# Performance work log

Hardware: AMD Instinct MI355X
Metric: run time of the kernel (lower is better)

## Reference

```python
import jax, jax.numpy as jnp
import numpy as np

B, S, DM, H = 2, 2048, 1024, 16
D = DM // H  # head dim = 64


def setup_inputs() -> dict:
    key = jax.random.key(0)
    k1, k2, k3, k4, k5 = jax.random.split(key, 5)
    hidden_states = jax.random.normal(k1, (B, S, DM), dtype=jnp.float32)
    attention_mask = jnp.zeros((B, 1, S, S), dtype=jnp.float32)
    position_ids = jnp.broadcast_to(jnp.arange(S, dtype=jnp.int32), (B, S))
    # nn.Linear weights stored as (out, in); x @ W.T
    Wq = jax.random.normal(k2, (DM, DM), dtype=jnp.float32) * 0.02
    Wk = jax.random.normal(k3, (DM, DM), dtype=jnp.float32) * 0.02
    Wv = jax.random.normal(k4, (DM, DM), dtype=jnp.float32) * 0.02
    return {"hidden_states": hidden_states, "attention_mask": attention_mask,
            "position_ids": position_ids, "Wq": Wq, "Wk": Wk, "Wv": Wv}


def _rotate_half(x):
    h = x.shape[-1] // 2
    return jnp.concatenate((-x[..., h:], x[..., :h]), axis=-1)


def _rope_cos_sin(position_ids, dtype):
    # inv_freq: (D/2,)
    inv_freq = 1.0 / (10000.0 ** (jnp.arange(0, D, 2, dtype=jnp.float32) / D))
    # freqs: (B, S, D/2)
    freqs = position_ids.astype(jnp.float32)[:, :, None] * inv_freq[None, None, :]
    emb = jnp.concatenate((freqs, freqs), axis=-1)  # (B, S, D)
    return jnp.cos(emb).astype(dtype), jnp.sin(emb).astype(dtype)


def reference(hidden_states, attention_mask, position_ids, Wq, Wk, Wv):
    def split_heads(x):  # (B,S,DM) -> (B,H,S,D)
        return x.reshape(B, S, H, D).transpose(0, 2, 1, 3)

    q = split_heads(hidden_states @ Wq.T)
    k = split_heads(hidden_states @ Wk.T)
    v = split_heads(hidden_states @ Wv.T)

    q = q * (D ** -0.5)

    cos, sin = _rope_cos_sin(position_ids, q.dtype)
    cos = cos[:, None, :, :]  # unsqueeze head dim -> (B,1,S,D)
    sin = sin[:, None, :, :]
    q = q * cos + _rotate_half(q) * sin
    k = k * cos + _rotate_half(k) * sin

    # (B,H,S,S)
    scores = jnp.einsum('bhqd,bhkd->bhqk', q, k) + attention_mask
    probs = jax.nn.softmax(scores.astype(jnp.float32), axis=-1).astype(q.dtype)
    ctx = jnp.einsum('bhqk,bhkd->bhqd', probs, v)  # (B,H,S,D)
    ctx = ctx.transpose(0, 2, 1, 3).reshape(B, S, DM)
    return ctx
```

## Files before the change

kernel.cpp:

```cpp
#include <hip/hip_runtime.h>
#include <math.h>

#define B  2
#define S  2048
#define DM 1024
#define H  16
#define Dh 64
#define BH (B*H)

typedef short  bf16x8 __attribute__((ext_vector_type(8)));
typedef float  f32x4  __attribute__((ext_vector_type(4)));

__device__ __forceinline__ unsigned short f2bf(float f) {
    unsigned u = __float_as_uint(f);
    u = (u + 0x7fffu + ((u >> 16) & 1u)) >> 16;
    return (unsigned short)u;
}

__global__ __launch_bounds__(256) void cast_kernel(const float* __restrict__ X,
                                                   const float* __restrict__ Wq,
                                                   const float* __restrict__ Wk,
                                                   const float* __restrict__ Wv,
                                                   unsigned short* __restrict__ Xb,
                                                   unsigned short* __restrict__ Wb) {
    const long c = (long)(blockIdx.x * 256 + threadIdx.x) * 4;
    const float* src;
    unsigned short* dst;
    if (c < 4194304L) {
        src = X + c;  dst = Xb + c;
    } else {
        const long c2 = c - 4194304L;
        const int  wi = (int)(c2 >> 20);
        const long r  = c2 & 1048575L;
        src = (wi == 0 ? Wq : (wi == 1 ? Wk : Wv)) + r;
        dst = Wb + c2;
    }
    const float4 v = *(const float4*)src;
    ushort4 o;
    o.x = f2bf(v.x); o.y = f2bf(v.y); o.z = f2bf(v.z); o.w = f2bf(v.w);
    *(ushort4*)dst = o;
}

__device__ __forceinline__ void gload_lds16(const unsigned short* g, unsigned short* l) {
    __builtin_amdgcn_global_load_lds(
        (const __attribute__((address_space(1))) unsigned int*)g,
        (__attribute__((address_space(3))) unsigned int*)l,
        16, 0, 0);
}

__global__ __launch_bounds__(256) void qkv_gemm(const unsigned short* __restrict__ Xb,
                                                const unsigned short* __restrict__ Wb,
                                                const int* __restrict__ pos,
                                                unsigned short* __restrict__ Qb,
                                                unsigned short* __restrict__ Kb,
                                                unsigned short* __restrict__ Vb) {
    __shared__ __align__(16) unsigned short As[128 * 32];
    __shared__ __align__(16) unsigned short Bs[128 * 32];

    const int tid  = threadIdx.x;
    const int w    = tid >> 6;
    const int lane = tid & 63;
    const int col  = lane & 15;
    const int quad = lane >> 4;
    const int m0 = blockIdx.x * 128;
    const int n0 = blockIdx.y * 128;
    const int mw = (w & 1) * 64;
    const int nw = (w >> 1) * 64;

    const int srow = (lane >> 2);
    const int sk8  = (lane & 3) * 8;

    f32x4 acc[4][4] = {};

    for (int k0 = 0; k0 < 1024; k0 += 32) {
        __syncthreads();
        #pragma unroll
        for (int it = 0; it < 2; ++it) {
            const int rbase = w * 16 + it * 64;
            gload_lds16(Xb + (size_t)(m0 + rbase + srow) * 1024 + k0 + sk8,
                        &As[rbase * 32]);
            gload_lds16(Wb + (size_t)(n0 + rbase + srow) * 1024 + k0 + sk8,
                        &Bs[rbase * 32]);
        }
        __syncthreads();

        bf16x8 a[4], bb[4];
        #pragma unroll
        for (int i = 0; i < 4; ++i)
            a[i] = *(const bf16x8*)&As[(mw + i * 16 + col) * 32 + quad * 8];
        #pragma unroll
        for (int j = 0; j < 4; ++j)
            bb[j] = *(const bf16x8*)&Bs[(nw + j * 16 + col) * 32 + quad * 8];
        #pragma unroll
        for (int i = 0; i < 4; ++i)
            #pragma unroll
            for (int j = 0; j < 4; ++j)
                acc[i][j] = __builtin_amdgcn_mfma_f32_16x16x32_bf16(a[i], bb[j], acc[i][j], 0, 0, 0);
    }

    const int wsel   = n0 >> 10;
    const int base64 = (n0 & 1023) + nw;
    const int hh     = base64 >> 6;

    if (wsel == 2) {
        #pragma unroll
        for (int i = 0; i < 4; ++i) {
            const int ss0 = m0 + mw + i * 16 + quad * 4;
            const int bb2 = ss0 >> 11, ss = ss0 & 2047;
            #pragma unroll
            for (int j = 0; j < 4; ++j) {
                const int d = j * 16 + col;
                ushort4 ov;
                ov.x = f2bf(acc[i][j][0]); ov.y = f2bf(acc[i][j][1]);
                ov.z = f2bf(acc[i][j][2]); ov.w = f2bf(acc[i][j][3]);
                *(ushort4*)(Vb + ((size_t)(bb2 * H + hh) * Dh + d) * S + ss) = ov;
            }
        }
    } else {
        unsigned short* dp = (wsel == 0) ? Qb : Kb;
        const float qscale = (wsel == 0) ? 0.125f : 1.0f;
        const float inv0 = exp2f(-(float)col * 0.41524101186092029f);
        const float inv1 = exp2f(-(float)(col + 16) * 0.41524101186092029f);
        #pragma unroll
        for (int i = 0; i < 4; ++i) {
            #pragma unroll
            for (int r = 0; r < 4; ++r) {
                const int m   = m0 + mw + i * 16 + quad * 4 + r;
                const int bb2 = m >> 11, ss = m & 2047;
                const float p = (float)pos[bb2 * S + ss];
                float sn0, cs0, sn1, cs1;
                sincosf(p * inv0, &sn0, &cs0);
                sincosf(p * inv1, &sn1, &cs1);
                const float a0 = acc[i][0][r], a1 = acc[i][1][r];
                const float a2 = acc[i][2][r], a3 = acc[i][3][r];
                unsigned short* o = dp + ((size_t)(bb2 * H + hh) * S + ss) * Dh;
                o[col]      = f2bf((a0 * cs0 - a2 * sn0) * qscale);
                o[col + 16] = f2bf((a1 * cs1 - a3 * sn1) * qscale);
                o[col + 32] = f2bf((a2 * cs0 + a0 * sn0) * qscale);
                o[col + 48] = f2bf((a3 * cs1 + a1 * sn1) * qscale);
            }
        }
    }
}

#define KSd 72
#define SHIFT_C 8.0f
#define NT (S / 64)

__global__ __launch_bounds__(256) void attn_kernel(const unsigned short* __restrict__ Q,
                                                   const unsigned short* __restrict__ K,
                                                   const unsigned short* __restrict__ V,
                                                   const float* __restrict__ mask,
                                                   float* __restrict__ out) {
    __shared__ __align__(16) unsigned short Ks[2][64 * KSd];
    __shared__ __align__(16) unsigned short Vt[2][64 * KSd];
    __shared__ __align__(16) unsigned short Ps[4 * 32 * KSd];

    const int tid  = threadIdx.x;
    const int w    = tid >> 6;
    const int lane = tid & 63;
    const int col  = lane & 15;
    const int quad = lane >> 4;
    const int bh   = blockIdx.y;
    const int b    = bh >> 4, h = bh & 15;
    const int q0   = blockIdx.x * 128;
    const int qw   = q0 + w * 32;

    const int srow = tid >> 3;
    const int sc8  = (tid & 7) * 8;

    bf16x8 qa[2][2];
    #pragma unroll
    for (int u = 0; u < 2; ++u) {
        const unsigned short* qrow = Q + ((size_t)bh * S + qw + u * 16 + col) * Dh;
        qa[u][0] = *(const bf16x8*)(qrow + quad * 8);
        qa[u][1] = *(const bf16x8*)(qrow + 32 + quad * 8);
    }

    f32x4 o[4][2] = {};
    float lsum[2] = {0.f, 0.f};
    const float* mbase = mask + (size_t)b * S * S;
    unsigned short* pw = Ps + w * 32 * KSd;
    const unsigned short* Kbase = K + (size_t)bh * S * Dh;
    const unsigned short* Vbase = V + (size_t)bh * Dh * S;

    bf16x8 kp[2], vp[2];
    #pragma unroll
    for (int cc = 0; cc < 2; ++cc) {
        kp[cc] = *(const bf16x8*)(Kbase + (size_t)(srow + cc * 32) * Dh + sc8);
        vp[cc] = *(const bf16x8*)(Vbase + (size_t)(srow + cc * 32) * S + sc8);
    }
    #pragma unroll
    for (int cc = 0; cc < 2; ++cc) {
        const int row = srow + cc * 32;
        *(bf16x8*)&Ks[0][row * KSd + sc8] = kp[cc];
        *(bf16x8*)&Vt[0][row * KSd + sc8] = vp[cc];
    }
    __syncthreads();

    for (int kt = 0; kt < NT; ++kt) {
        const int cur = kt & 1;

        if (kt + 1 < NT) {
            #pragma unroll
            for (int cc = 0; cc < 2; ++cc) {
                kp[cc] = *(const bf16x8*)(Kbase + (size_t)((kt + 1) * 64 + srow + cc * 32) * Dh + sc8);
                vp[cc] = *(const bf16x8*)(Vbase + (size_t)(srow + cc * 32) * S + (kt + 1) * 64 + sc8);
            }
        }

        float4 mv[4][2];
        #pragma unroll
        for (int u = 0; u < 2; ++u)
            #pragma unroll
            for (int f = 0; f < 4; ++f)
                mv[f][u] = *(const float4*)(mbase + (size_t)(qw + u * 16 + col) * S
                                            + kt * 64 + f * 16 + quad * 4);

        f32x4 sc[4][2] = {};
        #pragma unroll
        for (int f = 0; f < 4; ++f) {
            const bf16x8 ka0 = *(const bf16x8*)&Ks[cur][(f * 16 + col) * KSd + quad * 8];
            const bf16x8 ka1 = *(const bf16x8*)&Ks[cur][(f * 16 + col) * KSd + 32 + quad * 8];
            #pragma unroll
            for (int u = 0; u < 2; ++u) {
                sc[f][u] = __builtin_amdgcn_mfma_f32_16x16x32_bf16(ka0, qa[u][0], sc[f][u], 0, 0, 0);
                sc[f][u] = __builtin_amdgcn_mfma_f32_16x16x32_bf16(ka1, qa[u][1], sc[f][u], 0, 0, 0);
            }
        }

        #pragma unroll
        for (int u = 0; u < 2; ++u) {
            #pragma unroll
            for (int f = 0; f < 4; ++f) {
                sc[f][u][0] += mv[f][u].x; sc[f][u][1] += mv[f][u].y;
                sc[f][u][2] += mv[f][u].z; sc[f][u][3] += mv[f][u].w;
            }
            #pragma unroll
            for (int f = 0; f < 4; ++f)
                #pragma unroll
                for (int r = 0; r < 4; ++r) {
                    const float pv = __expf(sc[f][u][r] - SHIFT_C);
                    sc[f][u][r] = pv;
                    lsum[u] += pv;
                }
            unsigned short* pq = pw + (u * 16 + col) * KSd;
            #pragma unroll
            for (int f = 0; f < 4; ++f) {
                const unsigned v0 = (unsigned)f2bf(sc[f][u][0]) | ((unsigned)f2bf(sc[f][u][1]) << 16);
                const unsigned v1 = (unsigned)f2bf(sc[f][u][2]) | ((unsigned)f2bf(sc[f][u][3]) << 16);
                *(uint2*)&pq[f * 16 + quad * 4] = make_uint2(v0, v1);
            }
        }

        if (kt + 1 < NT) {
            const int nxt = cur ^ 1;
            #pragma unroll
            for (int cc = 0; cc < 2; ++cc) {
                const int row = srow + cc * 32;
                *(bf16x8*)&Ks[nxt][row * KSd + sc8] = kp[cc];
                *(bf16x8*)&Vt[nxt][row * KSd + sc8] = vp[cc];
            }
        }
        __threadfence_block();

        #pragma unroll
        for (int kc = 0; kc < 2; ++kc) {
            bf16x8 pb[2];
            #pragma unroll
            for (int u = 0; u < 2; ++u)
                pb[u] = *(const bf16x8*)&pw[(u * 16 + col) * KSd + kc * 32 + quad * 8];
            #pragma unroll
            for (int g = 0; g < 4; ++g) {
                const bf16x8 va = *(const bf16x8*)&Vt[cur][(g * 16 + col) * KSd + kc * 32 + quad * 8];
                #pragma unroll
                for (int u = 0; u < 2; ++u)
                    o[g][u] = __builtin_amdgcn_mfma_f32_16x16x32_bf16(va, pb[u], o[g][u], 0, 0, 0);
            }
        }
        __syncthreads();
    }

    #pragma unroll
    for (int u = 0; u < 2; ++u) {
        lsum[u] += __shfl_xor(lsum[u], 16, 64);
        lsum[u] += __shfl_xor(lsum[u], 32, 64);
    }

    #pragma unroll
    for (int u = 0; u < 2; ++u) {
        const float inv = 1.f / lsum[u];
        float* op = out + ((size_t)b * S + qw + u * 16 + col) * DM + h * Dh + quad * 4;
        #pragma unroll
        for (int g = 0; g < 4; ++g) {
            float4 ov;
            ov.x = o[g][u][0] * inv; ov.y = o[g][u][1] * inv;
            ov.z = o[g][u][2] * inv; ov.w = o[g][u][3] * inv;
            *(float4*)(op + g * 16) = ov;
        }
    }
}

extern "C" void kernel_launch(void* const* d_in, const int* in_sizes, int n_in,
                              void* d_out, int out_size, void* d_ws, size_t ws_size,
                              hipStream_t stream) {
    const float* hs   = (const float*)d_in[0];
    const float* mask = (const float*)d_in[1];
    const int*   pos  = (const int*)  d_in[2];
    const float* Wq   = (const float*)d_in[3];
    const float* Wk   = (const float*)d_in[4];
    const float* Wv   = (const float*)d_in[5];
    float* out = (float*)d_out;

    unsigned short* Xb = (unsigned short*)d_ws;
    unsigned short* Wb = Xb + 4194304;
    unsigned short* Qb = Wb + 3145728;
    unsigned short* Kb = Qb + 4194304;
    unsigned short* Vb = Kb + 4194304;

    cast_kernel<<<7168, 256, 0, stream>>>(hs, Wq, Wk, Wv, Xb, Wb);
    qkv_gemm<<<dim3(32, 24), 256, 0, stream>>>(Xb, Wb, pos, Qb, Kb, Vb);
    attn_kernel<<<dim3(S / 128, BH), 256, 0, stream>>>(Qb, Kb, Vb, mask, out);
}
```

Before: 228.7 us.

## Precompute RoPE table, stage GEMM epilogue through LDS, swizzle tiles, prefetch mask

Moves the RoPE sin/cos computation into a separate small kernel that writes a cos/sin table, which the QKV GEMM epilogue then reads instead of calling sincosf per element. The epilogue now stages outputs in shared memory so Q/K/V are written with coalesced 16-byte stores rather than scattered 2-byte or strided stores. It also XOR-swizzles the GEMM LDS tiles to reduce bank conflicts, and prefetches the attention mask one tile ahead. The cost is extra LDS, added barriers, an extra kernel launch and a table in workspace.

```diff
diff --git a/kernel.cpp b/kernel.cpp
--- a/kernel.cpp
+++ b/kernel.cpp
@@ -41,6 +41,18 @@
     *(ushort4*)dst = o;
 }
 
+__global__ __launch_bounds__(256) void rope_tab_kernel(const int* __restrict__ pos,
+                                                       float* __restrict__ Tab) {
+    const int idx = blockIdx.x * 256 + threadIdx.x;
+    const int i  = idx & 31;
+    const int bs = idx >> 5;
+    const float p   = (float)pos[bs];
+    const float inv = exp2f(-(float)i * 0.41524101186092029f);
+    float sn, cs;
+    sincosf(p * inv, &sn, &cs);
+    ((float2*)Tab)[idx] = make_float2(cs, sn);
+}
+
 __device__ __forceinline__ void gload_lds16(const unsigned short* g, unsigned short* l) {
     __builtin_amdgcn_global_load_lds(
         (const __attribute__((address_space(1))) unsigned int*)g,
@@ -50,12 +62,13 @@
 
 __global__ __launch_bounds__(256) void qkv_gemm(const unsigned short* __restrict__ Xb,
                                                 const unsigned short* __restrict__ Wb,
-                                                const int* __restrict__ pos,
+                                                const float* __restrict__ Tab,
                                                 unsigned short* __restrict__ Qb,
                                                 unsigned short* __restrict__ Kb,
                                                 unsigned short* __restrict__ Vb) {
     __shared__ __align__(16) unsigned short As[128 * 32];
     __shared__ __align__(16) unsigned short Bs[128 * 32];
+    __shared__ __align__(16) unsigned short Es[64 * 136];
 
     const int tid  = threadIdx.x;
     const int w    = tid >> 6;
@@ -67,8 +80,8 @@
     const int mw = (w & 1) * 64;
     const int nw = (w >> 1) * 64;
 
-    const int srow = (lane >> 2);
-    const int sk8  = (lane & 3) * 8;
+    const int srow = lane >> 2;
+    const int sk8  = (((lane & 3) ^ (srow & 3))) * 8;
 
     f32x4 acc[4][4] = {};
 
@@ -84,13 +97,14 @@
         }
         __syncthreads();
 
+        const int fs = (quad ^ (col & 3)) * 8;
         bf16x8 a[4], bb[4];
         #pragma unroll
         for (int i = 0; i < 4; ++i)
-            a[i] = *(const bf16x8*)&As[(mw + i * 16 + col) * 32 + quad * 8];
+            a[i] = *(const bf16x8*)&As[(mw + i * 16 + col) * 32 + fs];
         #pragma unroll
         for (int j = 0; j < 4; ++j)
-            bb[j] = *(const bf16x8*)&Bs[(nw + j * 16 + col) * 32 + quad * 8];
+            bb[j] = *(const bf16x8*)&Bs[(nw + j * 16 + col) * 32 + fs];
         #pragma unroll
         for (int i = 0; i < 4; ++i)
             #pragma unroll
@@ -98,46 +112,75 @@
                 acc[i][j] = __builtin_amdgcn_mfma_f32_16x16x32_bf16(a[i], bb[j], acc[i][j], 0, 0, 0);
     }
 
-    const int wsel   = n0 >> 10;
-    const int base64 = (n0 & 1023) + nw;
-    const int hh     = base64 >> 6;
+    const int wsel = n0 >> 10;
+    const int hh0  = (n0 & 1023) >> 6;
+    const int bb2  = m0 >> 11;
+    const int ssb  = m0 & 2047;
 
     if (wsel == 2) {
         #pragma unroll
-        for (int i = 0; i < 4; ++i) {
-            const int ss0 = m0 + mw + i * 16 + quad * 4;
-            const int bb2 = ss0 >> 11, ss = ss0 & 2047;
-            #pragma unroll
-            for (int j = 0; j < 4; ++j) {
-                const int d = j * 16 + col;
-                ushort4 ov;
-                ov.x = f2bf(acc[i][j][0]); ov.y = f2bf(acc[i][j][1]);
-                ov.z = f2bf(acc[i][j][2]); ov.w = f2bf(acc[i][j][3]);
-                *(ushort4*)(Vb + ((size_t)(bb2 * H + hh) * Dh + d) * S + ss) = ov;
+        for (int half = 0; half < 2; ++half) {
+            __syncthreads();
+            if ((w >> 1) == half) {
+                #pragma unroll
+                for (int i = 0; i < 4; ++i) {
+                    const int sl = mw + i * 16 + quad * 4;
+                    #pragma unroll
+                    for (int j = 0; j < 4; ++j) {
+                        const int dl = j * 16 + col;
+                        ushort4 ov;
+                        ov.x = f2bf(acc[i][j][0]); ov.y = f2bf(acc[i][j][1]);
+                        ov.z = f2bf(acc[i][j][2]); ov.w = f2bf(acc[i][j][3]);
+                        *(ushort4*)&Es[dl * 136 + sl] = ov;
+                    }
+                }
+            }
+            __syncthreads();
+            #pragma unroll
+            for (int k = 0; k < 4; ++k) {
+                const int c  = tid + k * 256;
+                const int dl = c >> 4;
+                const int s8 = (c & 15) * 8;
+                const int d  = half * 64 + dl;
+                const bf16x8 v = *(const bf16x8*)&Es[dl * 136 + s8];
+                *(bf16x8*)(Vb + ((size_t)(bb2 * H + hh0 + (d >> 6)) * Dh + (d & 63)) * S
+                           + ssb + s8) = v;
             }
         }
     } else {
         unsigned short* dp = (wsel == 0) ? Qb : Kb;
         const float qscale = (wsel == 0) ? 0.125f : 1.0f;
-        const float inv0 = exp2f(-(float)col * 0.41524101186092029f);
-        const float inv1 = exp2f(-(float)(col + 16) * 0.41524101186092029f);
-        #pragma unroll
-        for (int i = 0; i < 4; ++i) {
-            #pragma unroll
-            for (int r = 0; r < 4; ++r) {
-                const int m   = m0 + mw + i * 16 + quad * 4 + r;
-                const int bb2 = m >> 11, ss = m & 2047;
-                const float p = (float)pos[bb2 * S + ss];
-                float sn0, cs0, sn1, cs1;
-                sincosf(p * inv0, &sn0, &cs0);
-                sincosf(p * inv1, &sn1, &cs1);
-                const float a0 = acc[i][0][r], a1 = acc[i][1][r];
-                const float a2 = acc[i][2][r], a3 = acc[i][3][r];
-                unsigned short* o = dp + ((size_t)(bb2 * H + hh) * S + ss) * Dh;
-                o[col]      = f2bf((a0 * cs0 - a2 * sn0) * qscale);
-                o[col + 16] = f2bf((a1 * cs1 - a3 * sn1) * qscale);
-                o[col + 32] = f2bf((a2 * cs0 + a0 * sn0) * qscale);
-                o[col + 48] = f2bf((a3 * cs1 + a1 * sn1) * qscale);
+        #pragma unroll
+        for (int half = 0; half < 2; ++half) {
+            __syncthreads();
+            if ((w & 1) == half) {
+                #pragma unroll
+                for (int i = 0; i < 4; ++i) {
+                    #pragma unroll
+                    for (int r = 0; r < 4; ++r) {
+                        const int rl = i * 16 + quad * 4 + r;
+                        const int ss = ssb + half * 64 + rl;
+                        const float2 t0 = ((const float2*)Tab)[(size_t)(bb2 * S + ss) * 32 + col];
+                        const float2 t1 = ((const float2*)Tab)[(size_t)(bb2 * S + ss) * 32 + col + 16];
+                        const float a0 = acc[i][0][r] * qscale, a1 = acc[i][1][r] * qscale;
+                        const float a2 = acc[i][2][r] * qscale, a3 = acc[i][3][r] * qscale;
+                        unsigned short* e = &Es[rl * 136 + nw];
+                        e[col]      = f2bf(a0 * t0.x - a2 * t0.y);
+                        e[col + 16] = f2bf(a1 * t1.x - a3 * t1.y);
+                        e[col + 32] = f2bf(a2 * t0.x + a0 * t0.y);
+                        e[col + 48] = f2bf(a3 * t1.x + a1 * t1.y);
+                    }
+                }
+            }
+            __syncthreads();
+            #pragma unroll
+            for (int k = 0; k < 4; ++k) {
+                const int c  = tid + k * 256;
+                const int rl = c >> 4;
+                const int d8 = (c & 15) * 8;
+                const bf16x8 v = *(const bf16x8*)&Es[rl * 136 + d8];
+                *(bf16x8*)(dp + ((size_t)(bb2 * H + hh0 + (d8 >> 6)) * S
+                                 + ssb + half * 64 + rl) * Dh + (d8 & 63)) = v;
             }
         }
     }
@@ -185,11 +228,18 @@
     const unsigned short* Vbase = V + (size_t)bh * Dh * S;
 
     bf16x8 kp[2], vp[2];
+    float4 mv[4][2];
     #pragma unroll
     for (int cc = 0; cc < 2; ++cc) {
         kp[cc] = *(const bf16x8*)(Kbase + (size_t)(srow + cc * 32) * Dh + sc8);
         vp[cc] = *(const bf16x8*)(Vbase + (size_t)(srow + cc * 32) * S + sc8);
     }
+    #pragma unroll
+    for (int u = 0; u < 2; ++u)
+        #pragma unroll
+        for (int f = 0; f < 4; ++f)
+            mv[f][u] = *(const float4*)(mbase + (size_t)(qw + u * 16 + col) * S
+                                        + f * 16 + quad * 4);
     #pragma unroll
     for (int cc = 0; cc < 2; ++cc) {
         const int row = srow + cc * 32;
@@ -201,21 +251,20 @@
     for (int kt = 0; kt < NT; ++kt) {
         const int cur = kt & 1;
 
+        float4 mvp[4][2];
         if (kt + 1 < NT) {
             #pragma unroll
             for (int cc = 0; cc < 2; ++cc) {
                 kp[cc] = *(const bf16x8*)(Kbase + (size_t)((kt + 1) * 64 + srow + cc * 32) * Dh + sc8);
                 vp[cc] = *(const bf16x8*)(Vbase + (size_t)(srow + cc * 32) * S + (kt + 1) * 64 + sc8);
             }
-        }
-
-        float4 mv[4][2];
-        #pragma unroll
-        for (int u = 0; u < 2; ++u)
-            #pragma unroll
-            for (int f = 0; f < 4; ++f)
-                mv[f][u] = *(const float4*)(mbase + (size_t)(qw + u * 16 + col) * S
-                                            + kt * 64 + f * 16 + quad * 4);
+            #pragma unroll
+            for (int u = 0; u < 2; ++u)
+                #pragma unroll
+                for (int f = 0; f < 4; ++f)
+                    mvp[f][u] = *(const float4*)(mbase + (size_t)(qw + u * 16 + col) * S
+                                                 + (kt + 1) * 64 + f * 16 + quad * 4);
+        }
 
         f32x4 sc[4][2] = {};
         #pragma unroll
@@ -254,6 +303,11 @@
         }
 
         if (kt + 1 < NT) {
+            #pragma unroll
+            for (int u = 0; u < 2; ++u)
+                #pragma unroll
+                for (int f = 0; f < 4; ++f)
+                    mv[f][u] = mvp[f][u];
             const int nxt = cur ^ 1;
             #pragma unroll
             for (int cc = 0; cc < 2; ++cc) {
@@ -317,8 +371,10 @@
     unsigned short* Qb = Wb + 3145728;
     unsigned short* Kb = Qb + 4194304;
     unsigned short* Vb = Kb + 4194304;
+    float*          Tab = (float*)(Vb + 4194304);
 
     cast_kernel<<<7168, 256, 0, stream>>>(hs, Wq, Wk, Wv, Xb, Wb);
-    qkv_gemm<<<dim3(32, 24), 256, 0, stream>>>(Xb, Wb, pos, Qb, Kb, Vb);
+    rope_tab_kernel<<<512, 256, 0, stream>>>(pos, Tab);
+    qkv_gemm<<<dim3(32, 24), 256, 0, stream>>>(Xb, Wb, Tab, Qb, Kb, Vb);
     attn_kernel<<<dim3(S / 128, BH), 256, 0, stream>>>(Qb, Kb, Vb, mask, out);
 }
```

New measurement: 226.6 us. About the same (-0.9%).
